# Kernel optimization log

Hardware: AMD Instinct MI355X
Metric: run time of the kernel (lower is better)

## Reference

```python
import jax, jax.numpy as jnp
import numpy as np

H = 12          # num attention heads
DH = 64         # head dim
D = H * DH      # hidden size = 768
B, S = 2, 2048


def setup_inputs() -> dict:
    key = jax.random.key(0)
    ks = jax.random.split(key, 8)
    scale = 1.0 / np.sqrt(D)
    return {
        "hidden_states": jax.random.normal(ks[0], (B, S, D), jnp.float32),
        "attention_mask": jnp.zeros((B, 1, 1, S), jnp.float32),
        "position_bias": jax.random.normal(ks[1], (1, H, S, S), jnp.float32) * 0.1,
        "Wq": jax.random.normal(ks[2], (D, D), jnp.float32) * scale,
        "bq": jnp.zeros((D,), jnp.float32),
        "Wk": jax.random.normal(ks[3], (D, D), jnp.float32) * scale,
        "bk": jnp.zeros((D,), jnp.float32),
        "Wv": jax.random.normal(ks[4], (D, D), jnp.float32) * scale,
        "bv": jnp.zeros((D,), jnp.float32),
        "Wo": jax.random.normal(ks[5], (D, D), jnp.float32) * scale,
        "bo": jnp.zeros((D,), jnp.float32),
    }


def reference(hidden_states, attention_mask, position_bias,
              Wq, bq, Wk, bk, Wv, bv, Wo, bo):
    b, s, d = hidden_states.shape
    # Linear projections, then split heads: [B, S, D] -> [B, H, S, DH]
    def split_heads(x):
        return x.reshape(b, s, H, DH).transpose(0, 2, 1, 3)

    q = split_heads(hidden_states @ Wq.T + bq)
    k = split_heads(hidden_states @ Wk.T + bk)
    v = split_heads(hidden_states @ Wv.T + bv)

    # scores: [B, H, S, S]
    scores = jnp.einsum('bhqd,bhkd->bhqk', q, k) / jnp.sqrt(jnp.float32(DH))
    scores = scores + position_bias + attention_mask
    probs = jax.nn.softmax(scores, axis=-1)
    # dropout prob = 0.0 -> identity

    c = jnp.einsum('bhqk,bhkd->bhqd', probs, v)       # [B, H, S, DH]
    c = c.transpose(0, 2, 1, 3).reshape(b, s, d)      # [B, S, D]
    o = c @ Wo.T + bo
    return o
```

## Files before the change

### kernel.cpp

```cpp
#include <hip/hip_runtime.h>

typedef _Float16 f16x8 __attribute__((ext_vector_type(8)));
typedef float f32x4 __attribute__((ext_vector_type(4)));

#define NH 12
#define SEQ 2048
#define DM 768
#define DH 64

__global__ __launch_bounds__(256) void cast_kernel(
    const float* __restrict__ X, const float* __restrict__ Wq,
    const float* __restrict__ Wk, const float* __restrict__ Wv,
    const float* __restrict__ Wo, _Float16* __restrict__ Xh,
    _Float16* __restrict__ Wall)
{
    size_t base = ((size_t)blockIdx.x * 256 + threadIdx.x) * 8;
    const size_t NX = 3145728, NW = 589824, TOT = NX + 4 * NW;
    if (base >= TOT) return;
    const float* src;
    _Float16* dst;
    if (base < NX) { src = X + base; dst = Xh + base; }
    else {
        size_t r = base - NX;
        int w = (int)(r / NW);
        size_t o = r - (size_t)w * NW;
        src = (w == 0 ? Wq : w == 1 ? Wk : w == 2 ? Wv : Wo) + o;
        dst = Wall + r;
    }
    float4 a = *reinterpret_cast<const float4*>(src);
    float4 b = *reinterpret_cast<const float4*>(src + 4);
    f16x8 h;
    h[0] = (_Float16)a.x; h[1] = (_Float16)a.y; h[2] = (_Float16)a.z; h[3] = (_Float16)a.w;
    h[4] = (_Float16)b.x; h[5] = (_Float16)b.y; h[6] = (_Float16)b.z; h[7] = (_Float16)b.w;
    *reinterpret_cast<f16x8*>(dst) = h;
}

__global__ __launch_bounds__(256) void gemm_kernel(
    const _Float16* __restrict__ A,
    const _Float16* __restrict__ Wbase,
    const float* __restrict__ b0, const float* __restrict__ b1,
    const float* __restrict__ b2,
    _Float16* __restrict__ outQKV, float* __restrict__ outF32, int is_out)
{
    __shared__ _Float16 Asm[128 * 64];
    __shared__ _Float16 Bsm[128 * 64];
    const int tid = threadIdx.x;
    const int m0 = blockIdx.x * 128, n0 = blockIdx.y * 128, z = blockIdx.z;
    const _Float16* Wp = Wbase + (size_t)z * 589824;
    const float* bias = (z == 0) ? b0 : (z == 1 ? b1 : b2);
    const int w = tid >> 6, lane = tid & 63, lr = lane & 15, lg = lane >> 4;
    const int wm = w >> 1, wn = w & 1;

    f32x4 acc[4][4] = {};
    for (int kt = 0; kt < 12; ++kt) {
        __syncthreads();
        #pragma unroll
        for (int i = 0; i < 4; ++i) {
            int c = tid + i * 256;
            int row = c >> 3, col = (c & 7) * 8;
            int sw = (row & 7) << 4;
            f16x8 av = *reinterpret_cast<const f16x8*>(A + (size_t)(m0 + row) * 768 + kt * 64 + col);
            *reinterpret_cast<f16x8*>((char*)Asm + ((row * 128 + col * 2) ^ sw)) = av;
            f16x8 bv = *reinterpret_cast<const f16x8*>(Wp + (size_t)(n0 + row) * 768 + kt * 64 + col);
            *reinterpret_cast<f16x8*>((char*)Bsm + ((row * 128 + col * 2) ^ sw)) = bv;
        }
        __syncthreads();
        #pragma unroll
        for (int kf = 0; kf < 2; ++kf) {
            f16x8 af[4], bf[4];
            #pragma unroll
            for (int mi = 0; mi < 4; ++mi) {
                int row = wm * 64 + mi * 16 + lr;
                af[mi] = *reinterpret_cast<const f16x8*>(
                    (char*)Asm + ((row * 128 + kf * 64 + lg * 16) ^ ((row & 7) << 4)));
            }
            #pragma unroll
            for (int nj = 0; nj < 4; ++nj) {
                int row = wn * 64 + nj * 16 + lr;
                bf[nj] = *reinterpret_cast<const f16x8*>(
                    (char*)Bsm + ((row * 128 + kf * 64 + lg * 16) ^ ((row & 7) << 4)));
            }
            #pragma unroll
            for (int mi = 0; mi < 4; ++mi)
                #pragma unroll
                for (int nj = 0; nj < 4; ++nj)
                    acc[mi][nj] = __builtin_amdgcn_mfma_f32_16x16x32_f16(
                        af[mi], bf[nj], acc[mi][nj], 0, 0, 0);
        }
    }
    #pragma unroll
    for (int mi = 0; mi < 4; ++mi) {
        #pragma unroll
        for (int nj = 0; nj < 4; ++nj) {
            #pragma unroll
            for (int r = 0; r < 4; ++r) {
                int gm = m0 + wm * 64 + mi * 16 + lg * 4 + r;
                int gn = n0 + wn * 64 + nj * 16 + lr;
                float v = acc[mi][nj][r] + bias[gn];
                if (!is_out) {
                    int bb = gm >> 11, s = gm & 2047, hh = gn >> 6, dd = gn & 63;
                    outQKV[(size_t)z * 3145728 +
                           ((((size_t)bb * NH + hh) * SEQ + s) * DH + dd)] = (_Float16)v;
                } else {
                    outF32[(size_t)gm * 768 + gn] = v;
                }
            }
        }
    }
}

__global__ __launch_bounds__(256) void attn_kernel(
    const _Float16* __restrict__ Qh, const _Float16* __restrict__ Kh,
    const _Float16* __restrict__ Vh, const float* __restrict__ pb,
    const float* __restrict__ mask, _Float16* __restrict__ ctx)
{
    __shared__ _Float16 Kl[64 * 72];
    __shared__ _Float16 Vt[64 * 72];
    __shared__ _Float16 Pl[4 * 16 * 72];
    const int tid = threadIdx.x, w = tid >> 6, lane = tid & 63;
    const int lr = lane & 15, lg = lane >> 4;
    const int q0 = blockIdx.x * 64, h = blockIdx.y, b = blockIdx.z;
    const size_t headoff = ((size_t)b * NH + h) * SEQ * DH;
    const _Float16* Qp = Qh + headoff;
    const _Float16* Kp = Kh + headoff;
    const _Float16* Vp = Vh + headoff;

    f16x8 qf[2];
    #pragma unroll
    for (int kf = 0; kf < 2; ++kf)
        qf[kf] = *reinterpret_cast<const f16x8*>(
            Qp + (size_t)(q0 + w * 16 + lr) * DH + kf * 32 + lg * 8);

    f32x4 oacc[4] = {};
    float m_r[4], l_r[4];
    #pragma unroll
    for (int r = 0; r < 4; ++r) { m_r[r] = -3.0e38f; l_r[r] = 0.f; }
    _Float16* Pw = Pl + w * 16 * 72;

    for (int kt0 = 0; kt0 < SEQ; kt0 += 64) {
        __syncthreads();
        #pragma unroll
        for (int i = 0; i < 2; ++i) {
            int c = tid + i * 256;
            int row = c >> 3, col = (c & 7) * 8;
            f16x8 kv = *reinterpret_cast<const f16x8*>(Kp + (size_t)kt0 * DH + c * 8);
            *reinterpret_cast<f16x8*>(&Kl[row * 72 + col]) = kv;
            f16x8 vv = *reinterpret_cast<const f16x8*>(Vp + (size_t)kt0 * DH + c * 8);
            #pragma unroll
            for (int j = 0; j < 8; ++j) Vt[(col + j) * 72 + row] = vv[j];
        }
        __syncthreads();

        f32x4 sc4[4] = {};
        #pragma unroll
        for (int cf = 0; cf < 4; ++cf) {
            #pragma unroll
            for (int kf = 0; kf < 2; ++kf) {
                f16x8 kb = *reinterpret_cast<const f16x8*>(
                    &Kl[(cf * 16 + lr) * 72 + kf * 32 + lg * 8]);
                sc4[cf] = __builtin_amdgcn_mfma_f32_16x16x32_f16(qf[kf], kb, sc4[cf], 0, 0, 0);
            }
        }
        float sv[4][4];
        #pragma unroll
        for (int cf = 0; cf < 4; ++cf) {
            int col = kt0 + cf * 16 + lr;
            float mk = mask[(size_t)b * SEQ + col];
            #pragma unroll
            for (int r = 0; r < 4; ++r) {
                int grow = q0 + w * 16 + lg * 4 + r;
                float pbv = pb[(size_t)h * SEQ * SEQ + (size_t)grow * SEQ + col];
                sv[cf][r] = sc4[cf][r] * 0.125f + pbv + mk;
            }
        }
        float tm[4], rs[4], scale[4];
        #pragma unroll
        for (int r = 0; r < 4; ++r) {
            float t = fmaxf(fmaxf(sv[0][r], sv[1][r]), fmaxf(sv[2][r], sv[3][r]));
            #pragma unroll
            for (int msk = 1; msk < 16; msk <<= 1) t = fmaxf(t, __shfl_xor(t, msk));
            float mn = fmaxf(m_r[r], t);
            scale[r] = __expf(m_r[r] - mn);
            m_r[r] = mn;
            rs[r] = 0.f;
        }
        #pragma unroll
        for (int cf = 0; cf < 4; ++cf)
            #pragma unroll
            for (int r = 0; r < 4; ++r) {
                float p = __expf(sv[cf][r] - m_r[r]);
                rs[r] += p;
                Pw[(lg * 4 + r) * 72 + cf * 16 + lr] = (_Float16)p;
            }
        #pragma unroll
        for (int r = 0; r < 4; ++r) {
            #pragma unroll
            for (int msk = 1; msk < 16; msk <<= 1) rs[r] += __shfl_xor(rs[r], msk);
            l_r[r] = l_r[r] * scale[r] + rs[r];
        }
        #pragma unroll
        for (int cf = 0; cf < 4; ++cf)
            #pragma unroll
            for (int r = 0; r < 4; ++r) oacc[cf][r] *= scale[r];

        #pragma unroll
        for (int kf = 0; kf < 2; ++kf) {
            f16x8 pa = *reinterpret_cast<const f16x8*>(&Pw[lr * 72 + kf * 32 + lg * 8]);
            #pragma unroll
            for (int cf = 0; cf < 4; ++cf) {
                f16x8 vb = *reinterpret_cast<const f16x8*>(
                    &Vt[(cf * 16 + lr) * 72 + kf * 32 + lg * 8]);
                oacc[cf] = __builtin_amdgcn_mfma_f32_16x16x32_f16(pa, vb, oacc[cf], 0, 0, 0);
            }
        }
    }
    #pragma unroll
    for (int r = 0; r < 4; ++r) {
        float inv = 1.0f / l_r[r];
        int grow = q0 + w * 16 + lg * 4 + r;
        #pragma unroll
        for (int cf = 0; cf < 4; ++cf)
            ctx[((size_t)b * SEQ + grow) * DM + h * DH + cf * 16 + lr] =
                (_Float16)(oacc[cf][r] * inv);
    }
}

extern "C" void kernel_launch(void* const* d_in, const int* in_sizes, int n_in,
                              void* d_out, int out_size, void* d_ws, size_t ws_size,
                              hipStream_t stream) {
    const float* X    = (const float*)d_in[0];
    const float* mask = (const float*)d_in[1];
    const float* pb   = (const float*)d_in[2];
    const float* Wq   = (const float*)d_in[3];
    const float* bq   = (const float*)d_in[4];
    const float* Wk   = (const float*)d_in[5];
    const float* bk   = (const float*)d_in[6];
    const float* Wv   = (const float*)d_in[7];
    const float* bv   = (const float*)d_in[8];
    const float* Wo   = (const float*)d_in[9];
    const float* bo   = (const float*)d_in[10];
    float* out = (float*)d_out;

    _Float16* Xh   = (_Float16*)d_ws;
    _Float16* Wall = Xh + 3145728;
    _Float16* QKV  = Wall + 4 * 589824;
    _Float16* ctx  = QKV + 3 * 3145728;

    cast_kernel<<<2688, 256, 0, stream>>>(X, Wq, Wk, Wv, Wo, Xh, Wall);
    gemm_kernel<<<dim3(32, 6, 3), 256, 0, stream>>>(
        Xh, Wall, bq, bk, bv, QKV, nullptr, 0);
    attn_kernel<<<dim3(32, 12, 2), 256, 0, stream>>>(
        QKV, QKV + 3145728, QKV + 2 * 3145728, pb, mask, ctx);
    gemm_kernel<<<dim3(32, 6, 1), 256, 0, stream>>>(
        ctx, Wall + 3 * 589824, bo, bo, bo, nullptr, out, 1);
}
```

Before: 199.8 us.

## Prefetch next K/V and bias tiles, swizzle LDS, remap blocks per XCD

The attention kernel now loads the next K/V tile and the next position-bias and mask values into registers while computing on the current tile, and writes them to LDS after the MFMA work so global latency overlaps with compute. LDS buffers drop the padding and use an XOR swizzle to avoid bank conflicts. Softmax switches to exp2 with log2e folded into the scale and bias. Blocks are remapped with a 1D grid so each XCD handles whole batch-head groups, aiming for better L2 reuse of K/V. This costs extra registers for the prefetched tile, which may lower occupancy.

```diff
diff --git a/kernel.cpp b/kernel.cpp
--- a/kernel.cpp
+++ b/kernel.cpp
@@ -114,16 +114,21 @@
     const _Float16* __restrict__ Vh, const float* __restrict__ pb,
     const float* __restrict__ mask, _Float16* __restrict__ ctx)
 {
-    __shared__ _Float16 Kl[64 * 72];
-    __shared__ _Float16 Vt[64 * 72];
-    __shared__ _Float16 Pl[4 * 16 * 72];
+    __shared__ _Float16 Kl[64 * 64];
+    __shared__ _Float16 Vt[64 * 64];
+    __shared__ _Float16 Pl[4 * 16 * 64];
     const int tid = threadIdx.x, w = tid >> 6, lane = tid & 63;
     const int lr = lane & 15, lg = lane >> 4;
-    const int q0 = blockIdx.x * 64, h = blockIdx.y, b = blockIdx.z;
+    const int lin = blockIdx.x;
+    const int xcd = lin & 7, idx = lin >> 3;
+    const int bh = xcd * 3 + (idx >> 5);
+    const int q0 = (idx & 31) << 6;
+    const int h = bh % NH, b = bh / NH;
     const size_t headoff = ((size_t)b * NH + h) * SEQ * DH;
     const _Float16* Qp = Qh + headoff;
     const _Float16* Kp = Kh + headoff;
     const _Float16* Vp = Vh + headoff;
+    const float L2E = 1.44269504f;
 
     f16x8 qf[2];
     #pragma unroll
@@ -131,25 +136,63 @@
         qf[kf] = *reinterpret_cast<const f16x8*>(
             Qp + (size_t)(q0 + w * 16 + lr) * DH + kf * 32 + lg * 8);
 
+    const float* pbr[4];
+    #pragma unroll
+    for (int r = 0; r < 4; ++r)
+        pbr[r] = pb + (size_t)h * SEQ * SEQ + (size_t)(q0 + w * 16 + lg * 4 + r) * SEQ;
+    const float* mrow = mask + (size_t)b * SEQ;
+
     f32x4 oacc[4] = {};
     float m_r[4], l_r[4];
     #pragma unroll
     for (int r = 0; r < 4; ++r) { m_r[r] = -3.0e38f; l_r[r] = 0.f; }
-    _Float16* Pw = Pl + w * 16 * 72;
+    char* Pw = (char*)Pl + w * 2048;
+
+    const int c0 = tid, c1 = tid + 256;
+    const int row0 = c0 >> 3, col0 = (c0 & 7) << 3;
+    const int row1 = c1 >> 3, col1 = (c1 & 7) << 3;
+    f16x8 kn[2], vn[2];
+
+    kn[0] = *reinterpret_cast<const f16x8*>(Kp + c0 * 8);
+    kn[1] = *reinterpret_cast<const f16x8*>(Kp + c1 * 8);
+    vn[0] = *reinterpret_cast<const f16x8*>(Vp + c0 * 8);
+    vn[1] = *reinterpret_cast<const f16x8*>(Vp + c1 * 8);
+    float pbc[4][4];
+    #pragma unroll
+    for (int cf = 0; cf < 4; ++cf) {
+        float mk = mrow[cf * 16 + lr];
+        #pragma unroll
+        for (int r = 0; r < 4; ++r)
+            pbc[cf][r] = (pbr[r][cf * 16 + lr] + mk) * L2E;
+    }
+    #pragma unroll
+    for (int i = 0; i < 2; ++i) {
+        int row = i ? row1 : row0, col = i ? col1 : col0;
+        *reinterpret_cast<f16x8*>(
+            (char*)Kl + ((row * 128 + col * 2) ^ ((row & 7) << 4))) = kn[i];
+        #pragma unroll
+        for (int j = 0; j < 8; ++j) {
+            int d = col + j;
+            *reinterpret_cast<_Float16*>(
+                (char*)Vt + ((d * 128 + row * 2) ^ ((((d & 7) ^ ((d >> 3) & 7))) << 4))) = vn[i][j];
+        }
+    }
+    __syncthreads();
 
     for (int kt0 = 0; kt0 < SEQ; kt0 += 64) {
-        __syncthreads();
-        #pragma unroll
-        for (int i = 0; i < 2; ++i) {
-            int c = tid + i * 256;
-            int row = c >> 3, col = (c & 7) * 8;
-            f16x8 kv = *reinterpret_cast<const f16x8*>(Kp + (size_t)kt0 * DH + c * 8);
-            *reinterpret_cast<f16x8*>(&Kl[row * 72 + col]) = kv;
-            f16x8 vv = *reinterpret_cast<const f16x8*>(Vp + (size_t)kt0 * DH + c * 8);
-            #pragma unroll
-            for (int j = 0; j < 8; ++j) Vt[(col + j) * 72 + row] = vv[j];
-        }
-        __syncthreads();
+        const int nt = (kt0 + 64 < SEQ) ? kt0 + 64 : kt0;
+        kn[0] = *reinterpret_cast<const f16x8*>(Kp + (size_t)nt * DH + c0 * 8);
+        kn[1] = *reinterpret_cast<const f16x8*>(Kp + (size_t)nt * DH + c1 * 8);
+        vn[0] = *reinterpret_cast<const f16x8*>(Vp + (size_t)nt * DH + c0 * 8);
+        vn[1] = *reinterpret_cast<const f16x8*>(Vp + (size_t)nt * DH + c1 * 8);
+        float pbn[4][4];
+        #pragma unroll
+        for (int cf = 0; cf < 4; ++cf) {
+            float mk = mrow[nt + cf * 16 + lr];
+            #pragma unroll
+            for (int r = 0; r < 4; ++r)
+                pbn[cf][r] = (pbr[r][nt + cf * 16 + lr] + mk) * L2E;
+        }
 
         f32x4 sc4[4] = {};
         #pragma unroll
@@ -157,30 +200,25 @@
             #pragma unroll
             for (int kf = 0; kf < 2; ++kf) {
                 f16x8 kb = *reinterpret_cast<const f16x8*>(
-                    &Kl[(cf * 16 + lr) * 72 + kf * 32 + lg * 8]);
+                    (char*)Kl + (((cf * 16 + lr) * 128 + kf * 64 + lg * 16) ^ ((lr & 7) << 4)));
                 sc4[cf] = __builtin_amdgcn_mfma_f32_16x16x32_f16(qf[kf], kb, sc4[cf], 0, 0, 0);
             }
         }
         float sv[4][4];
         #pragma unroll
-        for (int cf = 0; cf < 4; ++cf) {
-            int col = kt0 + cf * 16 + lr;
-            float mk = mask[(size_t)b * SEQ + col];
-            #pragma unroll
-            for (int r = 0; r < 4; ++r) {
-                int grow = q0 + w * 16 + lg * 4 + r;
-                float pbv = pb[(size_t)h * SEQ * SEQ + (size_t)grow * SEQ + col];
-                sv[cf][r] = sc4[cf][r] * 0.125f + pbv + mk;
-            }
-        }
-        float tm[4], rs[4], scale[4];
+        for (int cf = 0; cf < 4; ++cf)
+            #pragma unroll
+            for (int r = 0; r < 4; ++r)
+                sv[cf][r] = sc4[cf][r] * 0.18033688f + pbc[cf][r];
+
+        float rs[4], scale[4];
         #pragma unroll
         for (int r = 0; r < 4; ++r) {
             float t = fmaxf(fmaxf(sv[0][r], sv[1][r]), fmaxf(sv[2][r], sv[3][r]));
             #pragma unroll
             for (int msk = 1; msk < 16; msk <<= 1) t = fmaxf(t, __shfl_xor(t, msk));
             float mn = fmaxf(m_r[r], t);
-            scale[r] = __expf(m_r[r] - mn);
+            scale[r] = exp2f(m_r[r] - mn);
             m_r[r] = mn;
             rs[r] = 0.f;
         }
@@ -188,9 +226,11 @@
         for (int cf = 0; cf < 4; ++cf)
             #pragma unroll
             for (int r = 0; r < 4; ++r) {
-                float p = __expf(sv[cf][r] - m_r[r]);
+                float p = exp2f(sv[cf][r] - m_r[r]);
                 rs[r] += p;
-                Pw[(lg * 4 + r) * 72 + cf * 16 + lr] = (_Float16)p;
+                int prow = lg * 4 + r;
+                *reinterpret_cast<_Float16*>(
+                    Pw + ((prow * 128 + (cf * 16 + lr) * 2) ^ ((prow & 7) << 4))) = (_Float16)p;
             }
         #pragma unroll
         for (int r = 0; r < 4; ++r) {
@@ -205,15 +245,37 @@
 
         #pragma unroll
         for (int kf = 0; kf < 2; ++kf) {
-            f16x8 pa = *reinterpret_cast<const f16x8*>(&Pw[lr * 72 + kf * 32 + lg * 8]);
+            f16x8 pa = *reinterpret_cast<const f16x8*>(
+                Pw + ((lr * 128 + kf * 64 + lg * 16) ^ ((lr & 7) << 4)));
             #pragma unroll
             for (int cf = 0; cf < 4; ++cf) {
+                int d = cf * 16 + lr;
                 f16x8 vb = *reinterpret_cast<const f16x8*>(
-                    &Vt[(cf * 16 + lr) * 72 + kf * 32 + lg * 8]);
+                    (char*)Vt + ((d * 128 + kf * 64 + lg * 16) ^ ((((d & 7) ^ ((d >> 3) & 7))) << 4)));
                 oacc[cf] = __builtin_amdgcn_mfma_f32_16x16x32_f16(pa, vb, oacc[cf], 0, 0, 0);
             }
         }
-    }
+
+        __syncthreads();
+        #pragma unroll
+        for (int i = 0; i < 2; ++i) {
+            int row = i ? row1 : row0, col = i ? col1 : col0;
+            *reinterpret_cast<f16x8*>(
+                (char*)Kl + ((row * 128 + col * 2) ^ ((row & 7) << 4))) = kn[i];
+            #pragma unroll
+            for (int j = 0; j < 8; ++j) {
+                int d = col + j;
+                *reinterpret_cast<_Float16*>(
+                    (char*)Vt + ((d * 128 + row * 2) ^ ((((d & 7) ^ ((d >> 3) & 7))) << 4))) = vn[i][j];
+            }
+        }
+        #pragma unroll
+        for (int cf = 0; cf < 4; ++cf)
+            #pragma unroll
+            for (int r = 0; r < 4; ++r) pbc[cf][r] = pbn[cf][r];
+        __syncthreads();
+    }
+
     #pragma unroll
     for (int r = 0; r < 4; ++r) {
         float inv = 1.0f / l_r[r];
@@ -249,7 +311,7 @@
     cast_kernel<<<2688, 256, 0, stream>>>(X, Wq, Wk, Wv, Wo, Xh, Wall);
     gemm_kernel<<<dim3(32, 6, 3), 256, 0, stream>>>(
         Xh, Wall, bq, bk, bv, QKV, nullptr, 0);
-    attn_kernel<<<dim3(32, 12, 2), 256, 0, stream>>>(
+    attn_kernel<<<768, 256, 0, stream>>>(
         QKV, QKV + 3145728, QKV + 2 * 3145728, pb, mask, ctx);
     gemm_kernel<<<dim3(32, 6, 1), 256, 0, stream>>>(
         ctx, Wall + 3 * 589824, bo, bo, bo, nullptr, out, 1);
```

Measured after the change: 192.1 us. 3.8% less time.

## Restructure attention: stage position bias in LDS, pre-transpose V, exp2 softmax

Applied to the files above, without the earlier changes.

The QKV GEMM now writes V already transposed, so the attention kernel reads V^T straight from global memory and no longer transposes it in LDS. The position bias is loaded in coalesced 512-column slabs into swizzled LDS as fp16 pre-scaled by log2(e), replacing strided per-element global reads. K is read directly from global memory into registers, and the MFMA operands are swapped so each lane owns one query row; this leaves a single max/sum per lane and allows exp2f with a folded scale. The grid is remapped so each XCD handles whole heads, with launch bounds set for two blocks per CU. Rounding the bias to fp16 adds precision loss, and K/V are now fetched from global or L2 without block-level sharing.

```diff
diff --git a/kernel.cpp b/kernel.cpp
--- a/kernel.cpp
+++ b/kernel.cpp
@@ -1,12 +1,15 @@
 #include <hip/hip_runtime.h>
 
 typedef _Float16 f16x8 __attribute__((ext_vector_type(8)));
+typedef _Float16 f16x4 __attribute__((ext_vector_type(4)));
 typedef float f32x4 __attribute__((ext_vector_type(4)));
 
 #define NH 12
 #define SEQ 2048
 #define DM 768
 #define DH 64
+
+#define SWZB(row, bo) ((row) * 1024 + ((bo) ^ (((row) & 7) << 4) ^ ((((bo) >> 8) & 3) << 4)))
 
 __global__ __launch_bounds__(256) void cast_kernel(
     const float* __restrict__ X, const float* __restrict__ Wq,
@@ -40,7 +43,8 @@
     const _Float16* __restrict__ Wbase,
     const float* __restrict__ b0, const float* __restrict__ b1,
     const float* __restrict__ b2,
-    _Float16* __restrict__ outQKV, float* __restrict__ outF32, int is_out)
+    _Float16* __restrict__ outQKV, _Float16* __restrict__ outVT,
+    float* __restrict__ outF32, int is_out)
 {
     __shared__ _Float16 Asm[128 * 64];
     __shared__ _Float16 Bsm[128 * 64];
@@ -99,8 +103,11 @@
                 float v = acc[mi][nj][r] + bias[gn];
                 if (!is_out) {
                     int bb = gm >> 11, s = gm & 2047, hh = gn >> 6, dd = gn & 63;
-                    outQKV[(size_t)z * 3145728 +
-                           ((((size_t)bb * NH + hh) * SEQ + s) * DH + dd)] = (_Float16)v;
+                    if (z == 2)
+                        outVT[(((size_t)bb * NH + hh) * DH + dd) * SEQ + s] = (_Float16)v;
+                    else
+                        outQKV[(size_t)z * 3145728 +
+                               ((((size_t)bb * NH + hh) * SEQ + s) * DH + dd)] = (_Float16)v;
                 } else {
                     outF32[(size_t)gm * 768 + gn] = v;
                 }
@@ -109,119 +116,162 @@
     }
 }
 
-__global__ __launch_bounds__(256) void attn_kernel(
+__global__ __launch_bounds__(256, 2) void attn_kernel(
     const _Float16* __restrict__ Qh, const _Float16* __restrict__ Kh,
-    const _Float16* __restrict__ Vh, const float* __restrict__ pb,
+    const _Float16* __restrict__ VTg, const float* __restrict__ pb,
     const float* __restrict__ mask, _Float16* __restrict__ ctx)
 {
-    __shared__ _Float16 Kl[64 * 72];
-    __shared__ _Float16 Vt[64 * 72];
-    __shared__ _Float16 Pl[4 * 16 * 72];
+    __shared__ _Float16 pbL[64 * 512];
+    __shared__ _Float16 Pl[4 * 16 * 64];
     const int tid = threadIdx.x, w = tid >> 6, lane = tid & 63;
     const int lr = lane & 15, lg = lane >> 4;
-    const int q0 = blockIdx.x * 64, h = blockIdx.y, b = blockIdx.z;
-    const size_t headoff = ((size_t)b * NH + h) * SEQ * DH;
+    const int lin = blockIdx.x;
+    const int xcd = lin & 7, idx = lin >> 3;
+    const int bh = xcd * 3 + idx / 32;
+    const int q0 = (idx & 31) << 6;
+    const int h = bh % NH, b = bh / NH;
+    const size_t headoff = (size_t)bh * SEQ * DH;
     const _Float16* Qp = Qh + headoff;
     const _Float16* Kp = Kh + headoff;
-    const _Float16* Vp = Vh + headoff;
-
-    f16x8 qf[2];
+    const _Float16* VTp = VTg + headoff;
+    const float L2E = 1.44269504f;
+
+    f16x8 qfr[2];
     #pragma unroll
     for (int kf = 0; kf < 2; ++kf)
-        qf[kf] = *reinterpret_cast<const f16x8*>(
+        qfr[kf] = *reinterpret_cast<const f16x8*>(
             Qp + (size_t)(q0 + w * 16 + lr) * DH + kf * 32 + lg * 8);
 
+    const int srow = tid >> 2;
+    const int scol = (tid & 3) * 128;
+    const float* psrc = pb + (size_t)h * SEQ * SEQ + (size_t)(q0 + srow) * SEQ + scol;
+    const float* mrow = mask + (size_t)b * SEQ;
+
     f32x4 oacc[4] = {};
-    float m_r[4], l_r[4];
-    #pragma unroll
-    for (int r = 0; r < 4; ++r) { m_r[r] = -3.0e38f; l_r[r] = 0.f; }
-    _Float16* Pw = Pl + w * 16 * 72;
-
-    for (int kt0 = 0; kt0 < SEQ; kt0 += 64) {
+    float m_r = -3.0e38f, l_r = 0.f;
+    char* pbB = (char*)pbL;
+    char* Pw = (char*)Pl + w * 2048;
+
+    for (int ss = 0; ss < 4; ++ss) {
         __syncthreads();
-        #pragma unroll
-        for (int i = 0; i < 2; ++i) {
-            int c = tid + i * 256;
-            int row = c >> 3, col = (c & 7) * 8;
-            f16x8 kv = *reinterpret_cast<const f16x8*>(Kp + (size_t)kt0 * DH + c * 8);
-            *reinterpret_cast<f16x8*>(&Kl[row * 72 + col]) = kv;
-            f16x8 vv = *reinterpret_cast<const f16x8*>(Vp + (size_t)kt0 * DH + c * 8);
-            #pragma unroll
-            for (int j = 0; j < 8; ++j) Vt[(col + j) * 72 + row] = vv[j];
+        {
+            const float* s0 = psrc + ss * 512;
+            f32x4 ca = *(const f32x4*)(s0 + 0);
+            f32x4 cb = *(const f32x4*)(s0 + 4);
+            f32x4 cc = *(const f32x4*)(s0 + 8);
+            f32x4 cd = *(const f32x4*)(s0 + 12);
+            #pragma unroll
+            for (int j = 0; j < 8; ++j) {
+                f32x4 na = {}, nb = {}, nc = {}, nd = {};
+                if (j < 7) {
+                    const float* sj = s0 + (j + 1) * 16;
+                    na = *(const f32x4*)(sj + 0);
+                    nb = *(const f32x4*)(sj + 4);
+                    nc = *(const f32x4*)(sj + 8);
+                    nd = *(const f32x4*)(sj + 12);
+                }
+                f16x8 lo, hi;
+                #pragma unroll
+                for (int i = 0; i < 4; ++i) {
+                    lo[i]     = (_Float16)(ca[i] * L2E);
+                    lo[4 + i] = (_Float16)(cb[i] * L2E);
+                    hi[i]     = (_Float16)(cc[i] * L2E);
+                    hi[4 + i] = (_Float16)(cd[i] * L2E);
+                }
+                int bo = (scol + j * 16) * 2;
+                *reinterpret_cast<f16x8*>(pbB + SWZB(srow, bo)) = lo;
+                *reinterpret_cast<f16x8*>(pbB + SWZB(srow, bo + 16)) = hi;
+                ca = na; cb = nb; cc = nc; cd = nd;
+            }
         }
         __syncthreads();
 
-        f32x4 sc4[4] = {};
-        #pragma unroll
-        for (int cf = 0; cf < 4; ++cf) {
+        for (int it = 0; it < 8; ++it) {
+            const int ktl = it * 64;
+            const int ktg = ss * 512 + ktl;
+
+            f16x8 ka[4][2];
+            #pragma unroll
+            for (int cf = 0; cf < 4; ++cf)
+                #pragma unroll
+                for (int kf = 0; kf < 2; ++kf)
+                    ka[cf][kf] = *reinterpret_cast<const f16x8*>(
+                        Kp + (size_t)(ktg + cf * 16 + lr) * DH + kf * 32 + lg * 8);
+            f32x4 sc[4] = {};
+            #pragma unroll
+            for (int cf = 0; cf < 4; ++cf)
+                #pragma unroll
+                for (int kf = 0; kf < 2; ++kf)
+                    sc[cf] = __builtin_amdgcn_mfma_f32_16x16x32_f16(
+                        ka[cf][kf], qfr[kf], sc[cf], 0, 0, 0);
+
+            float sv[4][4];
+            #pragma unroll
+            for (int cf = 0; cf < 4; ++cf) {
+                f16x4 pq = *reinterpret_cast<const f16x4*>(
+                    pbB + SWZB(w * 16 + lr, (ktl + cf * 16 + lg * 4) * 2));
+                f32x4 mk = *(const f32x4*)(mrow + ktg + cf * 16 + lg * 4);
+                #pragma unroll
+                for (int r = 0; r < 4; ++r)
+                    sv[cf][r] = sc[cf][r] * 0.18033688f + (float)pq[r] + mk[r] * L2E;
+            }
+
+            float t = sv[0][0];
+            #pragma unroll
+            for (int cf = 0; cf < 4; ++cf)
+                #pragma unroll
+                for (int r = 0; r < 4; ++r) t = fmaxf(t, sv[cf][r]);
+            t = fmaxf(t, __shfl_xor(t, 16));
+            t = fmaxf(t, __shfl_xor(t, 32));
+            float mn = fmaxf(m_r, t);
+            float sscale = exp2f(m_r - mn);
+            m_r = mn;
+            float rs = 0.f;
+            #pragma unroll
+            for (int cf = 0; cf < 4; ++cf) {
+                f16x4 pv;
+                #pragma unroll
+                for (int r = 0; r < 4; ++r) {
+                    float p = exp2f(sv[cf][r] - mn);
+                    rs += p;
+                    pv[r] = (_Float16)p;
+                }
+                *reinterpret_cast<f16x4*>(
+                    Pw + ((lr * 128 + cf * 32 + lg * 8) ^ ((lr & 7) << 4))) = pv;
+            }
+            rs += __shfl_xor(rs, 16);
+            rs += __shfl_xor(rs, 32);
+            l_r = l_r * sscale + rs;
+            f32x4 scv = {__shfl(sscale, lg * 4 + 0), __shfl(sscale, lg * 4 + 1),
+                         __shfl(sscale, lg * 4 + 2), __shfl(sscale, lg * 4 + 3)};
+            #pragma unroll
+            for (int cf = 0; cf < 4; ++cf) oacc[cf] *= scv;
+
             #pragma unroll
             for (int kf = 0; kf < 2; ++kf) {
-                f16x8 kb = *reinterpret_cast<const f16x8*>(
-                    &Kl[(cf * 16 + lr) * 72 + kf * 32 + lg * 8]);
-                sc4[cf] = __builtin_amdgcn_mfma_f32_16x16x32_f16(qf[kf], kb, sc4[cf], 0, 0, 0);
-            }
-        }
-        float sv[4][4];
-        #pragma unroll
-        for (int cf = 0; cf < 4; ++cf) {
-            int col = kt0 + cf * 16 + lr;
-            float mk = mask[(size_t)b * SEQ + col];
-            #pragma unroll
-            for (int r = 0; r < 4; ++r) {
-                int grow = q0 + w * 16 + lg * 4 + r;
-                float pbv = pb[(size_t)h * SEQ * SEQ + (size_t)grow * SEQ + col];
-                sv[cf][r] = sc4[cf][r] * 0.125f + pbv + mk;
-            }
-        }
-        float tm[4], rs[4], scale[4];
-        #pragma unroll
-        for (int r = 0; r < 4; ++r) {
-            float t = fmaxf(fmaxf(sv[0][r], sv[1][r]), fmaxf(sv[2][r], sv[3][r]));
-            #pragma unroll
-            for (int msk = 1; msk < 16; msk <<= 1) t = fmaxf(t, __shfl_xor(t, msk));
-            float mn = fmaxf(m_r[r], t);
-            scale[r] = __expf(m_r[r] - mn);
-            m_r[r] = mn;
-            rs[r] = 0.f;
-        }
-        #pragma unroll
-        for (int cf = 0; cf < 4; ++cf)
-            #pragma unroll
-            for (int r = 0; r < 4; ++r) {
-                float p = __expf(sv[cf][r] - m_r[r]);
-                rs[r] += p;
-                Pw[(lg * 4 + r) * 72 + cf * 16 + lr] = (_Float16)p;
-            }
-        #pragma unroll
-        for (int r = 0; r < 4; ++r) {
-            #pragma unroll
-            for (int msk = 1; msk < 16; msk <<= 1) rs[r] += __shfl_xor(rs[r], msk);
-            l_r[r] = l_r[r] * scale[r] + rs[r];
-        }
-        #pragma unroll
-        for (int cf = 0; cf < 4; ++cf)
-            #pragma unroll
-            for (int r = 0; r < 4; ++r) oacc[cf][r] *= scale[r];
-
-        #pragma unroll
-        for (int kf = 0; kf < 2; ++kf) {
-            f16x8 pa = *reinterpret_cast<const f16x8*>(&Pw[lr * 72 + kf * 32 + lg * 8]);
-            #pragma unroll
-            for (int cf = 0; cf < 4; ++cf) {
-                f16x8 vb = *reinterpret_cast<const f16x8*>(
-                    &Vt[(cf * 16 + lr) * 72 + kf * 32 + lg * 8]);
-                oacc[cf] = __builtin_amdgcn_mfma_f32_16x16x32_f16(pa, vb, oacc[cf], 0, 0, 0);
-            }
-        }
-    }
+                f16x8 pa = *reinterpret_cast<const f16x8*>(
+                    Pw + ((lr * 128 + kf * 64 + lg * 16) ^ ((lr & 7) << 4)));
+                #pragma unroll
+                for (int cf = 0; cf < 4; ++cf) {
+                    f16x8 vb = *reinterpret_cast<const f16x8*>(
+                        VTp + (size_t)(cf * 16 + lr) * SEQ + ktg + kf * 32 + lg * 8);
+                    oacc[cf] = __builtin_amdgcn_mfma_f32_16x16x32_f16(
+                        pa, vb, oacc[cf], 0, 0, 0);
+                }
+            }
+        }
+    }
+
+    float linv = 1.0f / l_r;
+    f32x4 iv = {__shfl(linv, lg * 4 + 0), __shfl(linv, lg * 4 + 1),
+                __shfl(linv, lg * 4 + 2), __shfl(linv, lg * 4 + 3)};
     #pragma unroll
     for (int r = 0; r < 4; ++r) {
-        float inv = 1.0f / l_r[r];
         int grow = q0 + w * 16 + lg * 4 + r;
         #pragma unroll
         for (int cf = 0; cf < 4; ++cf)
             ctx[((size_t)b * SEQ + grow) * DM + h * DH + cf * 16 + lr] =
-                (_Float16)(oacc[cf][r] * inv);
+                (_Float16)(oacc[cf][r] * iv[r]);
     }
 }
 
@@ -243,14 +293,15 @@
 
     _Float16* Xh   = (_Float16*)d_ws;
     _Float16* Wall = Xh + 3145728;
-    _Float16* QKV  = Wall + 4 * 589824;
-    _Float16* ctx  = QKV + 3 * 3145728;
+    _Float16* QK   = Wall + 4 * 589824;
+    _Float16* VT   = QK + 2 * 3145728;
+    _Float16* ctx  = VT + 3145728;
 
     cast_kernel<<<2688, 256, 0, stream>>>(X, Wq, Wk, Wv, Wo, Xh, Wall);
     gemm_kernel<<<dim3(32, 6, 3), 256, 0, stream>>>(
-        Xh, Wall, bq, bk, bv, QKV, nullptr, 0);
-    attn_kernel<<<dim3(32, 12, 2), 256, 0, stream>>>(
-        QKV, QKV + 3145728, QKV + 2 * 3145728, pb, mask, ctx);
+        Xh, Wall, bq, bk, bv, QK, VT, nullptr, 0);
+    attn_kernel<<<768, 256, 0, stream>>>(
+        QK, QK + 3145728, VT, pb, mask, ctx);
     gemm_kernel<<<dim3(32, 6, 1), 256, 0, stream>>>(
-        ctx, Wall + 3 * 589824, bo, bo, bo, nullptr, out, 1);
+        ctx, Wall + 3 * 589824, bo, bo, bo, nullptr, nullptr, out, 1);
 }
```

After: 306.2 us. +53.3%, slower.
